# Kernel tuning notes

Measured on AMD Instinct MI355X. Metric: run time of the kernel, lower is better.

## Reference

```python
import jax, jax.numpy as jnp
import numpy as np

B = 1024
P = 8
D = 2048
NUM_IDS = 64
MARGIN = 0.3
EPS = 1e-12


def setup_inputs() -> dict:
    key = jax.random.key(0)
    k1, k2, k3 = jax.random.split(key, 3)
    feats = jax.random.normal(k1, (B, P * D), dtype=jnp.float32)
    labels = jax.random.randint(k2, (B,), 0, NUM_IDS, dtype=jnp.int64)
    subs = jax.random.randint(k3, (B,), 0, 2, dtype=jnp.int64)
    return {"feats": feats, "labels": labels, "subs": subs}


def reference(feats, labels, subs):
    b = feats.shape[0]
    f = feats.reshape(b, -1, D)  # [B, P, D]
    dt = f.dtype

    # Per-sample class centers via a single segment-mean pass
    # (equivalent to the original per-sample boolean-mask mean loop).
    seg_sum = jax.ops.segment_sum(f, labels, num_segments=NUM_IDS)  # [NUM_IDS, P, D]
    counts = jax.ops.segment_sum(jnp.ones((b,), dt), labels, num_segments=NUM_IDS)
    centers_by_id = seg_sum / jnp.maximum(counts, 1.0)[:, None, None]
    centers = centers_by_id[labels]  # [B, P, D]

    # dist_ap[i] = sum_p ||f[i,p] - center[i,p]||
    d_ap = jnp.sqrt(jnp.clip(jnp.sum((f - centers) ** 2, axis=-1), EPS, None)).sum(-1)  # [B]
    dist_ap = d_ap[:, None] + d_ap[None, :]  # [B, B]

    # pairwise_distance: dist_aa[i,j] = sum_p ||f[i,p] - f[j,p]||, via gemm trick
    sq = jnp.sum(f * f, axis=-1)  # [B, P]
    inner = jnp.einsum('ipd,jpd->ijp', f, f)  # [B, B, P]
    d2 = sq[:, None, :] + sq[None, :, :] - 2.0 * inner
    dist_aa = jnp.sqrt(jnp.clip(d2, EPS, None)).sum(-1)  # [B, B]

    # masked margin loss over negative (different-label) pairs
    mask = labels[:, None] != labels[None, :]  # [B, B] bool
    vals = jnp.clip(dist_ap - dist_aa + MARGIN, 0.0, None)
    maskf = mask.astype(dt)
    loss = jnp.sum(vals * maskf) / jnp.sum(maskf)
    return loss
```

## Files before the change

### kernel.cpp

```cpp
#include <hip/hip_runtime.h>
#include <hip/hip_bf16.h>

#define B_ 1024
#define P_ 8
#define D_ 2048
#define FD_ (P_ * D_)
#define NID 64
#define MARGIN_ 0.3f
#define EPS_ 1e-12f

typedef unsigned short u16;
typedef float float4_t __attribute__((ext_vector_type(4)));

#define AS1 __attribute__((address_space(1)))
#define AS3 __attribute__((address_space(3)))

__device__ __forceinline__ float bf2f(unsigned v) {
    unsigned x = v << 16;
    float f;
    __builtin_memcpy(&f, &x, 4);
    return f;
}

static const size_t OFF_COUNTS = 0;
static const size_t OFF_OFFS   = 256;
static const size_t OFF_PERM   = 512;
static const size_t OFF_NEG    = 4608;
static const size_t OFF_POS    = 8168;
static const size_t OFF_TICKET = 8172;
static const size_t OFF_S      = 8192;
static const size_t OFF_SQ     = 40960;
static const size_t OFF_DAP    = 73728;
static const size_t OFF_FB     = 131072;
static const size_t OFF_PD     = OFF_FB + (size_t)B_ * FD_;

__global__ void k_prep(const float* __restrict__ feats, const int* __restrict__ labels,
                       unsigned char* __restrict__ fb, float* __restrict__ sq,
                       float* countsf, int* offs, int* perm, float* negcnt) {
    int tid = threadIdx.x;
    if (blockIdx.x < B_) {
        int i = blockIdx.x;
        int p = tid >> 6, lane = tid & 63;
        const float* frow = feats + (size_t)i * FD_ + p * D_;
        unsigned char* brow = fb + (size_t)p * B_ * D_ + (size_t)i * D_;
        float s2 = 0.f;
#pragma unroll
        for (int ch = 0; ch < 8; ch++) {
            int d = ch * 256 + lane * 4;
            float4 f = *(const float4*)(frow + d);
            int pk = __builtin_amdgcn_cvt_pk_fp8_f32(f.x, f.y, 0, false);
            pk = __builtin_amdgcn_cvt_pk_fp8_f32(f.z, f.w, pk, true);
            *(unsigned int*)(brow + d) = (unsigned int)pk;
            s2 += f.x * f.x + f.y * f.y + f.z * f.z + f.w * f.w;
        }
        for (int o = 32; o; o >>= 1) s2 += __shfl_down(s2, o, 64);
        if (lane == 0) sq[i * P_ + p] = s2;
    } else {
        __shared__ int h[NID], o[NID], cur[NID];
        if (tid < NID) h[tid] = 0;
        __syncthreads();
        for (int i = tid; i < B_; i += 512) atomicAdd(&h[labels[i]], 1);
        __syncthreads();
        if (tid == 0) {
            int acc = 0;
            long long ss = 0;
            for (int c = 0; c < NID; c++) {
                o[c] = acc;
                acc += h[c];
                ss += (long long)h[c] * h[c];
            }
            *negcnt = (float)((long long)B_ * B_ - ss);
        }
        __syncthreads();
        if (tid < NID) {
            countsf[tid] = (float)h[tid];
            offs[tid] = o[tid];
            cur[tid] = o[tid];
        }
        __syncthreads();
        for (int i = tid; i < B_; i += 512) {
            int pos = atomicAdd(&cur[labels[i]], 1);
            perm[pos] = i;
        }
    }
}

__global__ __launch_bounds__(512, 4) void k_pairs(const unsigned char* __restrict__ fb,
                                                  const float* __restrict__ sq,
                                                  const int* __restrict__ labels,
                                                  float* __restrict__ S,
                                                  u16* __restrict__ pd) {
    const int p = blockIdx.x;
    int rem = blockIdx.y, ti = 0;
    while (rem >= 8 - ti) { rem -= 8 - ti; ti++; }
    const int tj = ti + rem;
    const int i0 = ti * 128, j0 = tj * 128;
    __shared__ __align__(16) unsigned char smem[65536];
    __shared__ float sqAs[128], sqBs[128];
    __shared__ int labA[128], labB[128];
    const int tid = threadIdx.x;
    const int lane = tid & 63, wid = tid >> 6;
    const int s = wid & 3, h = wid >> 2;
    if (tid < 128) {
        sqAs[tid] = sq[(i0 + tid) * 8 + p];
        labA[tid] = labels[i0 + tid];
    } else if (tid < 256) {
        int t = tid - 128;
        sqBs[t] = sq[(j0 + t) * 8 + p];
        labB[t] = labels[j0 + t];
    }

    const int wi = (s >> 1) * 64, wj = (s & 1) * 64;
    const int lhi = lane >> 4, llo = lane & 15;
    const int sl = llo & 7;
    const int lr = lane >> 3;
    const int lc = (lane & 7) ^ lr;

    unsigned char* const As = smem + h * 16384;
    unsigned char* const Bs = smem + 32768 + h * 16384;

    const size_t plbase = (size_t)p * ((size_t)B_ * D_);
    const size_t colbase = (size_t)h * 1024 + (size_t)lc * 16;
    const unsigned char* gA[4];
    const unsigned char* gB[4];
    unsigned char* lA[4];
    unsigned char* lB[4];
#pragma unroll
    for (int inst = 0; inst < 4; inst++) {
        int r0 = s * 32 + inst * 8;
        gA[inst] = fb + plbase + (size_t)(i0 + r0 + lr) * D_ + colbase;
        gB[inst] = fb + plbase + (size_t)(j0 + r0 + lr) * D_ + colbase;
        lA[inst] = As + r0 * 128;
        lB[inst] = Bs + r0 * 128;
    }

    float4_t acc[4][4];
#pragma unroll
    for (int a = 0; a < 4; a++)
#pragma unroll
        for (int b = 0; b < 4; b++) acc[a][b] = (float4_t){0.f, 0.f, 0.f, 0.f};

    for (int kb = 0; kb < 8; kb++) {
        const int koff = kb * 128;
        __syncthreads();
#pragma unroll
        for (int inst = 0; inst < 4; inst++) {
            __builtin_amdgcn_global_load_lds((const AS1 void*)(gA[inst] + koff),
                                             (AS3 void*)lA[inst], 16, 0, 0);
            __builtin_amdgcn_global_load_lds((const AS1 void*)(gB[inst] + koff),
                                             (AS3 void*)lB[inst], 16, 0, 0);
        }
        __syncthreads();
#pragma unroll
        for (int ks = 0; ks < 4; ks++) {
            const int pcb = ((2 * ks + (lhi >> 1)) ^ sl) * 16 + (lhi & 1) * 8;
            long af[4], bf[4];
#pragma unroll
            for (int a = 0; a < 4; a++) {
                af[a] = *(const long*)(As + (wi + a * 16 + llo) * 128 + pcb);
                bf[a] = *(const long*)(Bs + (wj + a * 16 + llo) * 128 + pcb);
            }
#pragma unroll
            for (int a = 0; a < 4; a++)
#pragma unroll
                for (int b = 0; b < 4; b++)
                    acc[a][b] = __builtin_amdgcn_mfma_f32_16x16x32_fp8_fp8(
                        af[a], bf[b], acc[a][b], 0, 0, 0);
        }
    }
    __syncthreads();
    float* ep = (float*)smem;
    if (h == 1) {
#pragma unroll
        for (int a = 0; a < 4; a++)
#pragma unroll
            for (int b = 0; b < 4; b++)
                *(float4_t*)&ep[(((s * 4 + a) * 4 + b) * 64 + lane) * 4] = acc[a][b];
    }
    __syncthreads();
    if (h == 0) {
        u16* outp = pd + (size_t)p * B_ * B_;
        float rs[4][4];
        float cs[4];
#pragma unroll
        for (int a = 0; a < 4; a++)
#pragma unroll
            for (int r = 0; r < 4; r++) rs[a][r] = 0.f;
#pragma unroll
        for (int b = 0; b < 4; b++) cs[b] = 0.f;
#pragma unroll
        for (int a = 0; a < 4; a++) {
            int la0 = labA[wi + a * 16 + lhi * 4 + 0];
            int la1 = labA[wi + a * 16 + lhi * 4 + 1];
            int la2 = labA[wi + a * 16 + lhi * 4 + 2];
            int la3 = labA[wi + a * 16 + lhi * 4 + 3];
#pragma unroll
            for (int b = 0; b < 4; b++) {
                float4_t o = *(const float4_t*)&ep[(((s * 4 + a) * 4 + b) * 64 + lane) * 4];
                int jl = wj + b * 16 + llo;
                int lb = labB[jl];
#pragma unroll
                for (int r = 0; r < 4; r++) {
                    int il = wi + a * 16 + lhi * 4 + r;
                    float t = acc[a][b][r] + o[r];
                    float d2 = sqAs[il] + sqBs[jl] - 2.0f * t;
                    outp[(size_t)(i0 + il) * B_ + (j0 + jl)] =
                        __bfloat16_as_ushort(__float2bfloat16(sqrtf(fmaxf(d2, EPS_))));
                    int la = (r == 0) ? la0 : (r == 1) ? la1 : (r == 2) ? la2 : la3;
                    if (lb == la) {
                        rs[a][r] += t;
                        cs[b] += t;
                    }
                }
            }
        }
#pragma unroll
        for (int a = 0; a < 4; a++)
#pragma unroll
            for (int r = 0; r < 4; r++) {
                float v = rs[a][r];
                v += __shfl_xor(v, 1, 64);
                v += __shfl_xor(v, 2, 64);
                v += __shfl_xor(v, 4, 64);
                v += __shfl_xor(v, 8, 64);
                if (llo == 0)
                    atomicAdd(&S[(size_t)(i0 + wi + a * 16 + lhi * 4 + r) * 8 + p], v);
            }
        if (tj > ti) {
#pragma unroll
            for (int b = 0; b < 4; b++) {
                float v = cs[b];
                v += __shfl_xor(v, 16, 64);
                v += __shfl_xor(v, 32, 64);
                if (lhi == 0)
                    atomicAdd(&S[(size_t)(j0 + wj + b * 16 + llo) * 8 + p], v);
            }
        }
    }
}

__global__ void k_dap(const float* __restrict__ S, const float* __restrict__ sq,
                      const float* __restrict__ countsf, const int* __restrict__ offs,
                      const int* __restrict__ perm, float* __restrict__ dap) {
    int c = blockIdx.x;
    int tid = threadIdx.x;
    int cnt = (int)countsf[c];
    int off = offs[c];
    __shared__ float T[8];
    if (tid < 8) {
        float t = 0.f;
        for (int m = 0; m < cnt; m++) t += S[(size_t)perm[off + m] * 8 + tid];
        T[tid] = t;
    }
    __syncthreads();
    float n = fmaxf((float)cnt, 1.f);
    float inv = 1.f / n, inv2 = inv * inv;
    for (int m = tid; m < cnt; m += 64) {
        int i = perm[off + m];
        float d = 0.f;
#pragma unroll
        for (int p = 0; p < 8; p++) {
            float d2 = sq[i * 8 + p] - 2.f * inv * S[(size_t)i * 8 + p] + inv2 * T[p];
            d += sqrtf(fmaxf(d2, EPS_));
        }
        dap[i] = d;
    }
}

__global__ void k_lossred(const u16* __restrict__ pd, const float* __restrict__ dap,
                          const int* __restrict__ labels, float* possum,
                          const float* negcnt, int* ticket, float* out) {
    int i = blockIdx.x;
    int tid = threadIdx.x;
    float di = dap[i];
    int li = labels[i];
    float lsum = 0.f;
    for (int j = i + 1 + tid; j < B_; j += 256) {
        if (labels[j] != li) {
            float daa = 0.f;
#pragma unroll
            for (int p = 0; p < 8; p++)
                daa += bf2f(pd[((size_t)p << 20) + (size_t)i * B_ + j]);
            lsum += fmaxf(di + dap[j] - daa + MARGIN_, 0.f);
        }
    }
    lsum *= 2.0f;
    for (int o = 32; o; o >>= 1) lsum += __shfl_down(lsum, o, 64);
    __shared__ float red[4];
    int wid = tid >> 6, lane = tid & 63;
    if (lane == 0) red[wid] = lsum;
    __syncthreads();
    if (tid == 0) {
        atomicAdd(possum, red[0] + red[1] + red[2] + red[3]);
        __threadfence();
        int t = atomicAdd(ticket, 1);
        if (t == B_ - 1) {
            float total = atomicAdd(possum, 0.0f);
            out[0] = total / negcnt[0];
        }
    }
}

extern "C" void kernel_launch(void* const* d_in, const int* in_sizes, int n_in,
                              void* d_out, int out_size, void* d_ws, size_t ws_size,
                              hipStream_t stream) {
    const float* feats = (const float*)d_in[0];
    const int* labels  = (const int*)d_in[1];
    float* out = (float*)d_out;

    char* w = (char*)d_ws;
    float* countsf = (float*)(w + OFF_COUNTS);
    int* offs      = (int*)(w + OFF_OFFS);
    int* perm      = (int*)(w + OFF_PERM);
    float* negcnt  = (float*)(w + OFF_NEG);
    float* possum  = (float*)(w + OFF_POS);
    int* ticket    = (int*)(w + OFF_TICKET);
    float* S       = (float*)(w + OFF_S);
    float* sq      = (float*)(w + OFF_SQ);
    float* dap     = (float*)(w + OFF_DAP);
    unsigned char* fb = (unsigned char*)(w + OFF_FB);
    u16* pd        = (u16*)(w + OFF_PD);

    hipMemsetAsync(w + OFF_POS, 0, (OFF_S - OFF_POS) + (size_t)B_ * P_ * 4, stream);

    k_prep<<<B_ + 1, 512, 0, stream>>>(feats, labels, fb, sq, countsf, offs, perm, negcnt);
    k_pairs<<<dim3(8, 36), 512, 0, stream>>>(fb, sq, labels, S, pd);
    k_dap<<<NID, 64, 0, stream>>>(S, sq, countsf, offs, perm, dap);
    k_lossred<<<B_, 256, 0, stream>>>(pd, dap, labels, possum, negcnt, ticket, out);
}
```

Baseline: 179.0 us.

## Pre-swizzle fp8 features into MFMA fragment order and drop LDS staging in GEMM

```diff
diff --git a/kernel.cpp b/kernel.cpp
--- a/kernel.cpp
+++ b/kernel.cpp
@@ -11,9 +11,6 @@
 
 typedef unsigned short u16;
 typedef float float4_t __attribute__((ext_vector_type(4)));
-
-#define AS1 __attribute__((address_space(1)))
-#define AS3 __attribute__((address_space(3)))
 
 __device__ __forceinline__ float bf2f(unsigned v) {
     unsigned x = v << 16;
@@ -34,32 +31,62 @@
 static const size_t OFF_FB     = 131072;
 static const size_t OFF_PD     = OFF_FB + (size_t)B_ * FD_;
 
+
 __global__ void k_prep(const float* __restrict__ feats, const int* __restrict__ labels,
                        unsigned char* __restrict__ fb, float* __restrict__ sq,
                        float* countsf, int* offs, int* perm, float* negcnt) {
     int tid = threadIdx.x;
-    if (blockIdx.x < B_) {
-        int i = blockIdx.x;
-        int p = tid >> 6, lane = tid & 63;
+    __shared__ __align__(16) unsigned char st[32768];
+    if (blockIdx.x < 512) {
+        const int p = blockIdx.x & 7;
+        const int rb = blockIdx.x >> 3;
+        const int r = tid >> 4;
+        const int s = tid & 15;
+        const int i = rb * 16 + r;
         const float* frow = feats + (size_t)i * FD_ + p * D_;
-        unsigned char* brow = fb + (size_t)p * B_ * D_ + (size_t)i * D_;
+        const int ks_lo = (s >> 1);
+        const int lhi0 = (s & 1) * 2;
         float s2 = 0.f;
 #pragma unroll
-        for (int ch = 0; ch < 8; ch++) {
-            int d = ch * 256 + lane * 4;
-            float4 f = *(const float4*)(frow + d);
-            int pk = __builtin_amdgcn_cvt_pk_fp8_f32(f.x, f.y, 0, false);
-            pk = __builtin_amdgcn_cvt_pk_fp8_f32(f.z, f.w, pk, true);
-            *(unsigned int*)(brow + d) = (unsigned int)pk;
-            s2 += f.x * f.x + f.y * f.y + f.z * f.z + f.w * f.w;
-        }
-        for (int o = 32; o; o >>= 1) s2 += __shfl_down(s2, o, 64);
-        if (lane == 0) sq[i * P_ + p] = s2;
+        for (int it = 0; it < 8; it++) {
+            int d = it * 256 + s * 16;
+            float4 f0 = *(const float4*)(frow + d);
+            float4 f1 = *(const float4*)(frow + d + 4);
+            float4 f2 = *(const float4*)(frow + d + 8);
+            float4 f3 = *(const float4*)(frow + d + 12);
+            s2 += f0.x*f0.x + f0.y*f0.y + f0.z*f0.z + f0.w*f0.w
+                + f1.x*f1.x + f1.y*f1.y + f1.z*f1.z + f1.w*f1.w
+                + f2.x*f2.x + f2.y*f2.y + f2.z*f2.z + f2.w*f2.w
+                + f3.x*f3.x + f3.y*f3.y + f3.z*f3.z + f3.w*f3.w;
+            unsigned u0 = (unsigned)__builtin_amdgcn_cvt_pk_fp8_f32(f0.x, f0.y, 0, false);
+            u0 = (unsigned)__builtin_amdgcn_cvt_pk_fp8_f32(f0.z, f0.w, (int)u0, true);
+            unsigned u1 = (unsigned)__builtin_amdgcn_cvt_pk_fp8_f32(f1.x, f1.y, 0, false);
+            u1 = (unsigned)__builtin_amdgcn_cvt_pk_fp8_f32(f1.z, f1.w, (int)u1, true);
+            unsigned u2 = (unsigned)__builtin_amdgcn_cvt_pk_fp8_f32(f2.x, f2.y, 0, false);
+            u2 = (unsigned)__builtin_amdgcn_cvt_pk_fp8_f32(f2.z, f2.w, (int)u2, true);
+            unsigned u3 = (unsigned)__builtin_amdgcn_cvt_pk_fp8_f32(f3.x, f3.y, 0, false);
+            u3 = (unsigned)__builtin_amdgcn_cvt_pk_fp8_f32(f3.z, f3.w, (int)u3, true);
+            int ks = it * 8 + ks_lo;
+            *(uint2*)&st[ks * 512 + lhi0 * 128 + r * 8] = make_uint2(u0, u1);
+            *(uint2*)&st[ks * 512 + (lhi0 + 1) * 128 + r * 8] = make_uint2(u2, u3);
+        }
+        s2 += __shfl_xor(s2, 1, 64);
+        s2 += __shfl_xor(s2, 2, 64);
+        s2 += __shfl_xor(s2, 4, 64);
+        s2 += __shfl_xor(s2, 8, 64);
+        if (s == 0) sq[i * 8 + p] = s2;
+        __syncthreads();
+        unsigned char* dst = fb + (size_t)p * 2097152 + (size_t)rb * 32768;
+#pragma unroll
+        for (int c = 0; c < 8; c++) {
+            int off = tid * 128 + c * 16;
+            *(uint4*)(dst + off) = *(const uint4*)&st[off];
+        }
     } else {
         __shared__ int h[NID], o[NID], cur[NID];
         if (tid < NID) h[tid] = 0;
         __syncthreads();
-        for (int i = tid; i < B_; i += 512) atomicAdd(&h[labels[i]], 1);
+        for (int i = tid; i < B_; i += 256) atomicAdd(&h[labels[i]], 1);
         __syncthreads();
         if (tid == 0) {
             int acc = 0;
@@ -78,60 +105,45 @@
             cur[tid] = o[tid];
         }
         __syncthreads();
-        for (int i = tid; i < B_; i += 512) {
+        for (int i = tid; i < B_; i += 256) {
             int pos = atomicAdd(&cur[labels[i]], 1);
             perm[pos] = i;
         }
     }
 }
 
-__global__ __launch_bounds__(512, 4) void k_pairs(const unsigned char* __restrict__ fb,
-                                                  const float* __restrict__ sq,
-                                                  const int* __restrict__ labels,
-                                                  float* __restrict__ S,
-                                                  u16* __restrict__ pd) {
+__global__ __launch_bounds__(128) void k_pairs(const unsigned char* __restrict__ fb,
+                                               const float* __restrict__ sq,
+                                               const int* __restrict__ labels,
+                                               float* __restrict__ S,
+                                               u16* __restrict__ pd) {
     const int p = blockIdx.x;
-    int rem = blockIdx.y, ti = 0;
-    while (rem >= 8 - ti) { rem -= 8 - ti; ti++; }
-    const int tj = ti + rem;
-    const int i0 = ti * 128, j0 = tj * 128;
-    __shared__ __align__(16) unsigned char smem[65536];
-    __shared__ float sqAs[128], sqBs[128];
-    __shared__ int labA[128], labB[128];
+    int rem = blockIdx.y, tu = 0;
+    while (rem >= 16 - tu) { rem -= 16 - tu; tu++; }
+    const int tv = tu + rem;
+    const int i0 = tu * 64, j0 = tv * 64;
+
+    __shared__ __align__(16) float ep[4096];
+    __shared__ float sqAs[64], sqBs[64];
+    __shared__ int labA[64], labB[64];
     const int tid = threadIdx.x;
-    const int lane = tid & 63, wid = tid >> 6;
-    const int s = wid & 3, h = wid >> 2;
-    if (tid < 128) {
+    const int lane = tid & 63;
+    const int h = tid >> 6;
+    if (tid < 64) {
         sqAs[tid] = sq[(i0 + tid) * 8 + p];
         labA[tid] = labels[i0 + tid];
-    } else if (tid < 256) {
-        int t = tid - 128;
-        sqBs[t] = sq[(j0 + t) * 8 + p];
-        labB[t] = labels[j0 + t];
-    }
-
-    const int wi = (s >> 1) * 64, wj = (s & 1) * 64;
-    const int lhi = lane >> 4, llo = lane & 15;
-    const int sl = llo & 7;
-    const int lr = lane >> 3;
-    const int lc = (lane & 7) ^ lr;
-
-    unsigned char* const As = smem + h * 16384;
-    unsigned char* const Bs = smem + 32768 + h * 16384;
-
-    const size_t plbase = (size_t)p * ((size_t)B_ * D_);
-    const size_t colbase = (size_t)h * 1024 + (size_t)lc * 16;
-    const unsigned char* gA[4];
-    const unsigned char* gB[4];
-    unsigned char* lA[4];
-    unsigned char* lB[4];
-#pragma unroll
-    for (int inst = 0; inst < 4; inst++) {
-        int r0 = s * 32 + inst * 8;
-        gA[inst] = fb + plbase + (size_t)(i0 + r0 + lr) * D_ + colbase;
-        gB[inst] = fb + plbase + (size_t)(j0 + r0 + lr) * D_ + colbase;
-        lA[inst] = As + r0 * 128;
-        lB[inst] = Bs + r0 * 128;
+    } else {
+        sqBs[lane] = sq[(j0 + lane) * 8 + p];
+        labB[lane] = labels[j0 + lane];
+    }
+
+    const unsigned char* base = fb + (size_t)p * 2097152 + (size_t)lane * 8;
+    const unsigned char* pA[4];
+    const unsigned char* pB[4];
+#pragma unroll
+    for (int a = 0; a < 4; a++) {
+        pA[a] = base + (size_t)(tu * 4 + a) * 32768 + (size_t)h * 32 * 512;
+        pB[a] = base + (size_t)(tv * 4 + a) * 32768 + (size_t)h * 32 * 512;
     }
 
     float4_t acc[4][4];
@@ -140,45 +152,33 @@
 #pragma unroll
         for (int b = 0; b < 4; b++) acc[a][b] = (float4_t){0.f, 0.f, 0.f, 0.f};
 
-    for (int kb = 0; kb < 8; kb++) {
-        const int koff = kb * 128;
-        __syncthreads();
-#pragma unroll
-        for (int inst = 0; inst < 4; inst++) {
-            __builtin_amdgcn_global_load_lds((const AS1 void*)(gA[inst] + koff),
-                                             (AS3 void*)lA[inst], 16, 0, 0);
-            __builtin_amdgcn_global_load_lds((const AS1 void*)(gB[inst] + koff),
-                                             (AS3 void*)lB[inst], 16, 0, 0);
-        }
-        __syncthreads();
-#pragma unroll
-        for (int ks = 0; ks < 4; ks++) {
-            const int pcb = ((2 * ks + (lhi >> 1)) ^ sl) * 16 + (lhi & 1) * 8;
-            long af[4], bf[4];
-#pragma unroll
-            for (int a = 0; a < 4; a++) {
-                af[a] = *(const long*)(As + (wi + a * 16 + llo) * 128 + pcb);
-                bf[a] = *(const long*)(Bs + (wj + a * 16 + llo) * 128 + pcb);
-            }
-#pragma unroll
-            for (int a = 0; a < 4; a++)
-#pragma unroll
-                for (int b = 0; b < 4; b++)
-                    acc[a][b] = __builtin_amdgcn_mfma_f32_16x16x32_fp8_fp8(
-                        af[a], bf[b], acc[a][b], 0, 0, 0);
-        }
-    }
-    __syncthreads();
-    float* ep = (float*)smem;
+#pragma unroll 4
+    for (int t = 0; t < 32; t++) {
+        const int koff = t * 512;
+        long af[4], bf[4];
+#pragma unroll
+        for (int a = 0; a < 4; a++) {
+            af[a] = *(const long*)(pA[a] + koff);
+            bf[a] = *(const long*)(pB[a] + koff);
+        }
+#pragma unroll
+        for (int a = 0; a < 4; a++)
+#pragma unroll
+            for (int b = 0; b < 4; b++)
+                acc[a][b] = __builtin_amdgcn_mfma_f32_16x16x32_fp8_fp8(
+                    af[a], bf[b], acc[a][b], 0, 0, 0);
+    }
+
     if (h == 1) {
 #pragma unroll
         for (int a = 0; a < 4; a++)
 #pragma unroll
             for (int b = 0; b < 4; b++)
-                *(float4_t*)&ep[(((s * 4 + a) * 4 + b) * 64 + lane) * 4] = acc[a][b];
+                *(float4_t*)&ep[((a * 4 + b) * 64 + lane) * 4] = acc[a][b];
     }
     __syncthreads();
     if (h == 0) {
+        const int lhi = lane >> 4, llo = lane & 15;
         u16* outp = pd + (size_t)p * B_ * B_;
         float rs[4][4];
         float cs[4];
@@ -190,18 +190,18 @@
         for (int b = 0; b < 4; b++) cs[b] = 0.f;
 #pragma unroll
         for (int a = 0; a < 4; a++) {
-            int la0 = labA[wi + a * 16 + lhi * 4 + 0];
-            int la1 = labA[wi + a * 16 + lhi * 4 + 1];
-            int la2 = labA[wi + a * 16 + lhi * 4 + 2];
-            int la3 = labA[wi + a * 16 + lhi * 4 + 3];
+            int la0 = labA[a * 16 + lhi * 4 + 0];
+            int la1 = labA[a * 16 + lhi * 4 + 1];
+            int la2 = labA[a * 16 + lhi * 4 + 2];
+            int la3 = labA[a * 16 + lhi * 4 + 3];
 #pragma unroll
             for (int b = 0; b < 4; b++) {
-                float4_t o = *(const float4_t*)&ep[(((s * 4 + a) * 4 + b) * 64 + lane) * 4];
-                int jl = wj + b * 16 + llo;
+                float4_t o = *(const float4_t*)&ep[((a * 4 + b) * 64 + lane) * 4];
+                int jl = b * 16 + llo;
                 int lb = labB[jl];
 #pragma unroll
                 for (int r = 0; r < 4; r++) {
-                    int il = wi + a * 16 + lhi * 4 + r;
+                    int il = a * 16 + lhi * 4 + r;
                     float t = acc[a][b][r] + o[r];
                     float d2 = sqAs[il] + sqBs[jl] - 2.0f * t;
                     outp[(size_t)(i0 + il) * B_ + (j0 + jl)] =
@@ -224,16 +224,16 @@
                 v += __shfl_xor(v, 4, 64);
                 v += __shfl_xor(v, 8, 64);
                 if (llo == 0)
-                    atomicAdd(&S[(size_t)(i0 + wi + a * 16 + lhi * 4 + r) * 8 + p], v);
+                    atomicAdd(&S[(size_t)(i0 + a * 16 + lhi * 4 + r) * 8 + p], v);
             }
-        if (tj > ti) {
+        if (tv > tu) {
 #pragma unroll
             for (int b = 0; b < 4; b++) {
                 float v = cs[b];
                 v += __shfl_xor(v, 16, 64);
                 v += __shfl_xor(v, 32, 64);
                 if (lhi == 0)
-                    atomicAdd(&S[(size_t)(j0 + wj + b * 16 + llo) * 8 + p], v);
+                    atomicAdd(&S[(size_t)(j0 + b * 16 + llo) * 8 + p], v);
             }
         }
     }
@@ -323,8 +323,8 @@
 
     hipMemsetAsync(w + OFF_POS, 0, (OFF_S - OFF_POS) + (size_t)B_ * P_ * 4, stream);
 
-    k_prep<<<B_ + 1, 512, 0, stream>>>(feats, labels, fb, sq, countsf, offs, perm, negcnt);
-    k_pairs<<<dim3(8, 36), 512, 0, stream>>>(fb, sq, labels, S, pd);
+    k_prep<<<513, 256, 0, stream>>>(feats, labels, fb, sq, countsf, offs, perm, negcnt);
+    k_pairs<<<dim3(8, 136), 128, 0, stream>>>(fb, sq, labels, S, pd);
     k_dap<<<NID, 64, 0, stream>>>(S, sq, countsf, offs, perm, dap);
     k_lossred<<<B_, 256, 0, stream>>>(pd, dap, labels, possum, negcnt, ticket, out);
 }
```

Result: slower. 196.3 us (+9.7%).
